# Kernel tuning notes

Measured on AMD Instinct MI355X. Metric: run time of the kernel, lower is better.

The kernel has to match this reference:

```python
import jax, jax.numpy as jnp
import numpy as np

N = 50000   # nodes
E = 800000  # edges (avg degree 16)
F = 96      # num_features
H = 96      # hidden_channels
G = 64      # graphs in batch
ALPHA = 0.5


def setup_inputs() -> dict:
    key = jax.random.key(0)
    ks = jax.random.split(key, 32)
    inp = {
        "x": jax.random.normal(ks[0], (N, F), jnp.float32),
        "edge_index": jax.random.randint(ks[1], (2, E), 0, N, dtype=jnp.int32),
        "batch": jnp.sort(jax.random.randint(ks[2], (N,), 0, G, dtype=jnp.int32)),
    }
    i = 3
    dims = [(F, H), (H, H), (H, H)]
    for l, (din, dout) in enumerate(dims, start=1):
        for tag in ("Wself", "Wsd", "Wds"):
            inp[f"{tag}{l}"] = jax.random.normal(ks[i], (din, dout), jnp.float32) * 0.05; i += 1
        for tag in ("bself", "bsd", "bds"):
            inp[f"{tag}{l}"] = jax.random.normal(ks[i], (dout,), jnp.float32) * 0.05; i += 1
    inp["lin1_w"] = jax.random.normal(ks[i], (H, 5), jnp.float32) * 0.05; i += 1
    inp["lin1_b"] = jax.random.normal(ks[i], (5,), jnp.float32) * 0.05; i += 1
    inp["lin2_w"] = jax.random.normal(ks[i], (5, 1), jnp.float32) * 0.05; i += 1
    inp["lin2_b"] = jax.random.normal(ks[i], (1,), jnp.float32) * 0.05
    return inp


def _agg_mean(x, idx_from, idx_to, n):
    # scatter-mean of x[idx_from] onto idx_to (PyG SAGEConv mean aggregation;
    # nodes with no incoming edges get 0)
    s = jax.ops.segment_sum(x[idx_from], idx_to, num_segments=n)
    c = jax.ops.segment_sum(jnp.ones((idx_to.shape[0],), x.dtype), idx_to, num_segments=n)
    return s / jnp.maximum(c, 1.0)[:, None]


def _dir_sage(x, src, dst, Wself, bself, Wsd, bsd, Wds, bds):
    n = x.shape[0]
    out_self = x @ Wself + bself
    # source_to_target: aggregate x[src] at dst; target_to_source: aggregate x[dst] at src
    out_sd = _agg_mean(x, src, dst, n) @ Wsd + bsd
    out_ds = _agg_mean(x, dst, src, n) @ Wds + bds
    return out_self + (1.0 - ALPHA) * out_sd + ALPHA * out_ds


def reference(x, edge_index, batch,
              Wself1, bself1, Wsd1, bsd1, Wds1, bds1,
              Wself2, bself2, Wsd2, bsd2, Wds2, bds2,
              Wself3, bself3, Wsd3, bsd3, Wds3, bds3,
              lin1_w, lin1_b, lin2_w, lin2_b):
    src, dst = edge_index[0], edge_index[1]
    h = jax.nn.relu(_dir_sage(x, src, dst, Wself1, bself1, Wsd1, bsd1, Wds1, bds1))
    h = jax.nn.relu(_dir_sage(h, src, dst, Wself2, bself2, Wsd2, bsd2, Wds2, bds2))
    h = jax.nn.relu(_dir_sage(h, src, dst, Wself3, bself3, Wsd3, bsd3, Wds3, bds3))
    g = jax.ops.segment_max(h, batch, num_segments=G)  # global_max_pool -> [G, H]
    g = jax.nn.relu(g @ lin1_w + lin1_b)
    return g @ lin2_w + lin2_b  # [G, 1]
```

## Files before the change

kernel.cpp:

```cpp
#include <hip/hip_runtime.h>
#include <hip/hip_bf16.h>

#define HF 96
#define GG 64
#define SB 64

typedef __attribute__((ext_vector_type(8))) short bf16x8;
typedef __attribute__((ext_vector_type(4))) float f32x4;

__device__ __forceinline__ unsigned short f2bf(float f) {
    unsigned u = __float_as_uint(f);
    unsigned r = (u + 0x7FFFu + ((u >> 16) & 1u)) >> 16;
    return (unsigned short)r;
}
__device__ __forceinline__ float bf2f(unsigned short h) {
    return __uint_as_float(((unsigned)h) << 16);
}

__global__ void count_kernel(const int* __restrict__ ei, int* __restrict__ cnt_dst,
                             int* __restrict__ cnt_src, int* __restrict__ slot_d,
                             int* __restrict__ slot_s, int E) {
    int e = blockIdx.x * blockDim.x + threadIdx.x;
    if (e >= E) return;
    int s = ei[e];
    int d = ei[E + e];
    slot_d[e] = atomicAdd(&cnt_dst[d], 1);
    slot_s[e] = atomicAdd(&cnt_src[s], 1);
}

__global__ __launch_bounds__(256) void scan_phase1(const int* __restrict__ cnt0,
                                                   const int* __restrict__ cnt1,
                                                   int* __restrict__ off0,
                                                   int* __restrict__ off1,
                                                   int* __restrict__ bsum, int N, int CH) {
    int dir = blockIdx.y;
    const int* cnt = dir ? cnt1 : cnt0;
    int* off = dir ? off1 : off0;
    int base = blockIdx.x * CH;
    int end = base + CH; if (end > N) end = N;
    __shared__ int buf[256];
    int carry = 0;
    for (int s = base; s < end; s += 256) {
        int i = s + threadIdx.x;
        int v = (i < end) ? cnt[i] : 0;
        buf[threadIdx.x] = v;
        __syncthreads();
        for (int st = 1; st < 256; st <<= 1) {
            int tv = (threadIdx.x >= st) ? buf[threadIdx.x - st] : 0;
            __syncthreads();
            buf[threadIdx.x] += tv;
            __syncthreads();
        }
        if (i < end) off[i] = carry + buf[threadIdx.x] - v;
        carry += buf[255];
        __syncthreads();
    }
    if (threadIdx.x == 0) bsum[dir * SB + blockIdx.x] = carry;
}

__global__ __launch_bounds__(64) void scan_phase2(int* __restrict__ bsum, int* __restrict__ boff,
                                                  int* __restrict__ off0, int* __restrict__ off1,
                                                  int N) {
    int dir = blockIdx.x;
    __shared__ int buf[SB];
    int v = bsum[dir * SB + threadIdx.x];
    buf[threadIdx.x] = v;
    __syncthreads();
    for (int st = 1; st < SB; st <<= 1) {
        int tv = (threadIdx.x >= st) ? buf[threadIdx.x - st] : 0;
        __syncthreads();
        buf[threadIdx.x] += tv;
        __syncthreads();
    }
    boff[dir * SB + threadIdx.x] = buf[threadIdx.x] - v;
    if (threadIdx.x == SB - 1) {
        int* off = dir ? off1 : off0;
        off[N] = buf[SB - 1];
    }
}

__global__ void scan_phase3(int* __restrict__ off0, int* __restrict__ off1,
                            const int* __restrict__ boff, int N, int CH) {
    int dir = blockIdx.y;
    int* off = dir ? off1 : off0;
    int i = blockIdx.x * 256 + threadIdx.x;
    if (i >= N) return;
    off[i] += boff[dir * SB + i / CH];
}

__global__ void fill_kernel(const int* __restrict__ ei, const int* __restrict__ off_dst,
                            const int* __restrict__ off_src, const int* __restrict__ slot_d,
                            const int* __restrict__ slot_s, int* __restrict__ nbr_dst,
                            int* __restrict__ nbr_src, int E) {
    int e = blockIdx.x * blockDim.x + threadIdx.x;
    if (e >= E) return;
    int s = ei[e];
    int d = ei[E + e];
    nbr_dst[off_dst[d] + slot_d[e]] = s;
    nbr_src[off_src[s] + slot_s[e]] = d;
}

__global__ void prep_kernel(const float* __restrict__ Wself, const float* __restrict__ Wsd,
                            const float* __restrict__ Wds, const float* __restrict__ bself,
                            const float* __restrict__ bsd, const float* __restrict__ bds,
                            unsigned short* __restrict__ Whi, unsigned short* __restrict__ Wlo,
                            float* __restrict__ bc) {
    int idx = blockIdx.x * 256 + threadIdx.x;
    if (idx < HF * 288) {
        int j = idx / 288;
        int kk = idx % 288;
        int m = kk / HF, k = kk % HF;
        const float* W = (m == 0) ? Wself : (m == 1) ? Wsd : Wds;
        float w = W[k * HF + j];
        unsigned short hi = f2bf(w);
        float rem = w - bf2f(hi);
        Whi[idx] = hi;
        Wlo[idx] = f2bf(rem);
    } else if (idx < HF * 288 + HF) {
        int j = idx - HF * 288;
        bc[j] = bself[j] + 0.5f * (bsd[j] + bds[j]);
    }
}

__global__ __launch_bounds__(256) void gather_kernel(
        const float* __restrict__ x,
        const int* __restrict__ off_dst, const int* __restrict__ nbr_dst,
        const int* __restrict__ off_src, const int* __restrict__ nbr_src,
        float* __restrict__ agg_sd, float* __restrict__ agg_ds, int N) {
    int t = blockIdx.x * blockDim.x + threadIdx.x;
    int n2 = t / 24;
    if (n2 >= 2 * N) return;
    int q = t % 24;
    int dir = (n2 >= N) ? 1 : 0;
    int n = n2 - dir * N;
    const int* off = dir ? off_src : off_dst;
    const int* nbr = dir ? nbr_src : nbr_dst;
    float* agg = dir ? agg_ds : agg_sd;

    int b = off[n], e = off[n + 1];
    const float* xq = x + q * 4;
    float4 a0 = make_float4(0.f, 0.f, 0.f, 0.f);
    float4 a1 = make_float4(0.f, 0.f, 0.f, 0.f);
    float4 a2 = make_float4(0.f, 0.f, 0.f, 0.f);
    float4 a3 = make_float4(0.f, 0.f, 0.f, 0.f);
    int i = b;
    for (; i + 4 <= e; i += 4) {
        int i0 = nbr[i + 0], i1 = nbr[i + 1], i2 = nbr[i + 2], i3 = nbr[i + 3];
        float4 v0 = *(const float4*)(xq + (long long)i0 * HF);
        float4 v1 = *(const float4*)(xq + (long long)i1 * HF);
        float4 v2 = *(const float4*)(xq + (long long)i2 * HF);
        float4 v3 = *(const float4*)(xq + (long long)i3 * HF);
        a0.x += v0.x; a0.y += v0.y; a0.z += v0.z; a0.w += v0.w;
        a1.x += v1.x; a1.y += v1.y; a1.z += v1.z; a1.w += v1.w;
        a2.x += v2.x; a2.y += v2.y; a2.z += v2.z; a2.w += v2.w;
        a3.x += v3.x; a3.y += v3.y; a3.z += v3.z; a3.w += v3.w;
    }
    for (; i < e; i++) {
        int i0 = nbr[i];
        float4 v0 = *(const float4*)(xq + (long long)i0 * HF);
        a0.x += v0.x; a0.y += v0.y; a0.z += v0.z; a0.w += v0.w;
    }
    float4 acc;
    acc.x = (a0.x + a1.x) + (a2.x + a3.x);
    acc.y = (a0.y + a1.y) + (a2.y + a3.y);
    acc.z = (a0.z + a1.z) + (a2.z + a3.z);
    acc.w = (a0.w + a1.w) + (a2.w + a3.w);
    float inv = 0.5f / fmaxf((float)(e - b), 1.0f);
    acc.x *= inv; acc.y *= inv; acc.z *= inv; acc.w *= inv;
    *(float4*)(agg + (long long)n * HF + q * 4) = acc;
}

#define LPAD 48
__global__ __launch_bounds__(256) void sage_mfma(
        const float* __restrict__ x, const float* __restrict__ agg_sd,
        const float* __restrict__ agg_ds,
        const unsigned short* __restrict__ Whi_g, const unsigned short* __restrict__ Wlo_g,
        const float* __restrict__ bc,
        float* __restrict__ out, int N) {
    __shared__ __align__(16) unsigned short Ahi[128 * LPAD];
    __shared__ __align__(16) unsigned short Alo[128 * LPAD];
    __shared__ __align__(16) unsigned short Whi[96 * LPAD];
    __shared__ __align__(16) unsigned short Wlo[96 * LPAD];

    const int tx = threadIdx.x;
    const int lane = tx & 63;
    const int wid = tx >> 6;
    const int wr = (wid >> 1) * 64;
    const int wc = (wid & 1) * 48;
    const int m = lane & 15;
    const int quad = lane >> 4;
    const int row0 = blockIdx.x * 128;

    const int arow = tx >> 1;
    const int ahalf = tx & 1;
    int argr = row0 + arow; if (argr > N - 1) argr = N - 1;

    f32x4 acc[4][3];
#pragma unroll
    for (int rt = 0; rt < 4; rt++)
#pragma unroll
        for (int ct = 0; ct < 3; ct++) acc[rt][ct] = (f32x4){0.f, 0.f, 0.f, 0.f};

    for (int kt = 0; kt < 9; kt++) {
        const float* A = (kt < 3) ? x : (kt < 6) ? agg_sd : agg_ds;
        const int koff = (kt % 3) * 32;
        const int kglob = kt * 32;

        {
            const float* Ar = A + (long long)argr * HF + koff + ahalf * 16;
            float4 v0 = *(const float4*)(Ar + 0);
            float4 v1 = *(const float4*)(Ar + 4);
            float4 v2 = *(const float4*)(Ar + 8);
            float4 v3 = *(const float4*)(Ar + 12);
            float f[16] = {v0.x, v0.y, v0.z, v0.w, v1.x, v1.y, v1.z, v1.w,
                           v2.x, v2.y, v2.z, v2.w, v3.x, v3.y, v3.z, v3.w};
            bf16x8 hv0, lv0, hv1, lv1;
#pragma unroll
            for (int i = 0; i < 8; i++) {
                unsigned short h = f2bf(f[i]);
                hv0[i] = (short)h;
                lv0[i] = (short)f2bf(f[i] - bf2f(h));
            }
#pragma unroll
            for (int i = 0; i < 8; i++) {
                unsigned short h = f2bf(f[8 + i]);
                hv1[i] = (short)h;
                lv1[i] = (short)f2bf(f[8 + i] - bf2f(h));
            }
            int base = arow * LPAD + ahalf * 16;
            *(bf16x8*)&Ahi[base + 0] = hv0;
            *(bf16x8*)&Ahi[base + 8] = hv1;
            *(bf16x8*)&Alo[base + 0] = lv0;
            *(bf16x8*)&Alo[base + 8] = lv1;
        }
        for (int s = tx; s < 384; s += 256) {
            int j = s >> 2, q2 = s & 3;
            long long go = (long long)j * 288 + kglob + q2 * 8;
            *(bf16x8*)&Whi[j * LPAD + q2 * 8] = *(const bf16x8*)(Whi_g + go);
            *(bf16x8*)&Wlo[j * LPAD + q2 * 8] = *(const bf16x8*)(Wlo_g + go);
        }
        __syncthreads();

        bf16x8 ah[4], al[4], bh[3], bl[3];
#pragma unroll
        for (int rt = 0; rt < 4; rt++) {
            int r = (wr + rt * 16 + m) * LPAD + quad * 8;
            ah[rt] = *(const bf16x8*)&Ahi[r];
            al[rt] = *(const bf16x8*)&Alo[r];
        }
#pragma unroll
        for (int ct = 0; ct < 3; ct++) {
            int r = (wc + ct * 16 + m) * LPAD + quad * 8;
            bh[ct] = *(const bf16x8*)&Whi[r];
            bl[ct] = *(const bf16x8*)&Wlo[r];
        }
#pragma unroll
        for (int rt = 0; rt < 4; rt++)
#pragma unroll
            for (int ct = 0; ct < 3; ct++) {
                acc[rt][ct] = __builtin_amdgcn_mfma_f32_16x16x32_bf16(ah[rt], bh[ct], acc[rt][ct], 0, 0, 0);
                acc[rt][ct] = __builtin_amdgcn_mfma_f32_16x16x32_bf16(ah[rt], bl[ct], acc[rt][ct], 0, 0, 0);
                acc[rt][ct] = __builtin_amdgcn_mfma_f32_16x16x32_bf16(al[rt], bh[ct], acc[rt][ct], 0, 0, 0);
            }
        __syncthreads();
    }

#pragma unroll
    for (int ct = 0; ct < 3; ct++) {
        int col = wc + ct * 16 + m;
        float bcv = bc[col];
#pragma unroll
        for (int rt = 0; rt < 4; rt++) {
#pragma unroll
            for (int reg = 0; reg < 4; reg++) {
                int r = row0 + wr + rt * 16 + quad * 4 + reg;
                if (r < N) out[(long long)r * HF + col] = fmaxf(acc[rt][ct][reg] + bcv, 0.f);
            }
        }
    }
}

#define POOL_CHUNK 128
__global__ void pool_kernel(const float* __restrict__ h, const int* __restrict__ batch,
                            unsigned* __restrict__ g, int N) {
    int j = threadIdx.x;
    if (j >= HF) return;
    int n0 = blockIdx.x * POOL_CHUNK;
    int end = n0 + POOL_CHUNK;
    if (end > N) end = N;
    float cur = 0.0f;
    int curb = -1;
    for (int n = n0; n < end; n++) {
        int b = batch[n];
        float v = h[(long long)n * HF + j];
        if (b != curb) {
            if (curb >= 0) atomicMax(&g[curb * HF + j], __float_as_uint(cur));
            curb = b;
            cur = v;
        } else {
            cur = fmaxf(cur, v);
        }
    }
    if (curb >= 0) atomicMax(&g[curb * HF + j], __float_as_uint(cur));
}

__global__ void mlp_kernel(const unsigned* __restrict__ g, const float* __restrict__ lin1_w,
                           const float* __restrict__ lin1_b, const float* __restrict__ lin2_w,
                           const float* __restrict__ lin2_b, float* __restrict__ out) {
    int gi = threadIdx.x;
    if (gi >= GG) return;
    float h5[5];
#pragma unroll
    for (int hh = 0; hh < 5; hh++) {
        float acc = lin1_b[hh];
#pragma unroll 8
        for (int k = 0; k < HF; k++)
            acc = fmaf(__uint_as_float(g[gi * HF + k]), lin1_w[k * 5 + hh], acc);
        h5[hh] = fmaxf(acc, 0.0f);
    }
    float o = lin2_b[0];
#pragma unroll
    for (int hh = 0; hh < 5; hh++) o = fmaf(h5[hh], lin2_w[hh * 1 + 0], o);
    out[gi] = o;
}

extern "C" void kernel_launch(void* const* d_in, const int* in_sizes, int n_in,
                              void* d_out, int out_size, void* d_ws, size_t ws_size,
                              hipStream_t stream) {
    const float* x     = (const float*)d_in[0];
    const int*   ei    = (const int*)d_in[1];
    const int*   batch = (const int*)d_in[2];
    const float* W[3][3];
    const float* B[3][3];
    for (int l = 0; l < 3; l++) {
        for (int t = 0; t < 3; t++) W[l][t] = (const float*)d_in[3 + l * 6 + t];
        for (int t = 0; t < 3; t++) B[l][t] = (const float*)d_in[3 + l * 6 + 3 + t];
    }
    const float* lin1_w = (const float*)d_in[21];
    const float* lin1_b = (const float*)d_in[22];
    const float* lin2_w = (const float*)d_in[23];
    const float* lin2_b = (const float*)d_in[24];

    const int N = in_sizes[0] / HF;
    const int E = in_sizes[1] / 2;

    float* hA      = (float*)d_ws;
    float* hB      = hA + (long long)N * HF;
    float* agg_sd  = hB + (long long)N * HF;
    float* agg_ds  = agg_sd + (long long)N * HF;
    int*   cnt_dst = (int*)(agg_ds + (long long)N * HF);
    int*   cnt_src = cnt_dst + N;
    int*   off_dst = cnt_src + N;
    int*   off_src = off_dst + (N + 1);
    int*   nbr_dst = off_src + (N + 1);
    int*   nbr_src = nbr_dst + E;
    int*   slot_d  = nbr_src + E;
    int*   slot_s  = slot_d + E;
    int*   bsum    = slot_s + E;
    int*   boff    = bsum + 2 * SB;
    float* bc3     = (float*)(boff + 2 * SB);
    uintptr_t p = (uintptr_t)(bc3 + 3 * HF);
    p = (p + 15) & ~(uintptr_t)15;
    unsigned short* Whi3 = (unsigned short*)p;
    unsigned short* Wlo3 = Whi3 + 3 * HF * 288;
    uintptr_t p2 = (uintptr_t)(Wlo3 + 3 * HF * 288);
    p2 = (p2 + 15) & ~(uintptr_t)15;
    unsigned* g = (unsigned*)p2;

    hipMemsetAsync(cnt_dst, 0, (size_t)2 * N * sizeof(int), stream);
    hipMemsetAsync(g, 0, (size_t)GG * HF * sizeof(unsigned), stream);

    const int prep_blocks = (HF * 288 + HF + 255) / 256;
    for (int l = 0; l < 3; l++)
        prep_kernel<<<prep_blocks, 256, 0, stream>>>(
            W[l][0], W[l][1], W[l][2], B[l][0], B[l][1], B[l][2],
            Whi3 + (long long)l * HF * 288, Wlo3 + (long long)l * HF * 288, bc3 + l * HF);

    const int CH = (N + SB - 1) / SB;
    count_kernel<<<(E + 255) / 256, 256, 0, stream>>>(ei, cnt_dst, cnt_src, slot_d, slot_s, E);
    scan_phase1<<<dim3(SB, 2), 256, 0, stream>>>(cnt_dst, cnt_src, off_dst, off_src, bsum, N, CH);
    scan_phase2<<<2, SB, 0, stream>>>(bsum, boff, off_dst, off_src, N);
    scan_phase3<<<dim3((N + 255) / 256, 2), 256, 0, stream>>>(off_dst, off_src, boff, N, CH);
    fill_kernel<<<(E + 255) / 256, 256, 0, stream>>>(ei, off_dst, off_src,
                                                     slot_d, slot_s, nbr_dst, nbr_src, E);

    const long long gather_threads = (long long)2 * N * 24;
    const int gather_blocks = (int)((gather_threads + 255) / 256);
    const int gemm_blocks = (N + 127) / 128;
    const int pool_blocks = (N + POOL_CHUNK - 1) / POOL_CHUNK;

    const float* cur_in = x;
    float* outs[3] = { hA, hB, hA };
    for (int l = 0; l < 3; l++) {
        gather_kernel<<<gather_blocks, 256, 0, stream>>>(
            cur_in, off_dst, nbr_dst, off_src, nbr_src, agg_sd, agg_ds, N);
        sage_mfma<<<gemm_blocks, 256, 0, stream>>>(
            cur_in, agg_sd, agg_ds,
            Whi3 + (long long)l * HF * 288, Wlo3 + (long long)l * HF * 288,
            bc3 + l * HF, outs[l], N);
        cur_in = outs[l];
    }

    pool_kernel<<<pool_blocks, 128, 0, stream>>>(outs[2], batch, g, N);
    mlp_kernel<<<1, 64, 0, stream>>>(g, lin1_w, lin1_b, lin2_w, lin2_b, (float*)d_out);
}
```

Before: 568.4 us.

## Remap gather threads to one node per lane with feature-slice blocks

The gather kernel changes from 24 threads per node, each summing a float4 slice, to one thread per (node, direction) pair. Blocks are split into 8 feature slices of 12 floats, each slice loaded as three float4s per neighbor. This cuts repeated neighbor-index and offset loads per node and lets consecutive blocks share slices of the same rows in cache. The cost is uncoalesced per-lane row accesses and lane divergence from differing degrees within a wavefront.

```diff
diff --git a/kernel.cpp b/kernel.cpp
--- a/kernel.cpp
+++ b/kernel.cpp
@@ -127,47 +127,60 @@
         const int* __restrict__ off_dst, const int* __restrict__ nbr_dst,
         const int* __restrict__ off_src, const int* __restrict__ nbr_src,
         float* __restrict__ agg_sd, float* __restrict__ agg_ds, int N) {
-    int t = blockIdx.x * blockDim.x + threadIdx.x;
-    int n2 = t / 24;
-    if (n2 >= 2 * N) return;
-    int q = t % 24;
-    int dir = (n2 >= N) ? 1 : 0;
-    int n = n2 - dir * N;
+    const int t8 = blockIdx.x & 7;
+    int pair = (blockIdx.x >> 3) * 256 + threadIdx.x;
+    if (pair >= 2 * N) return;
+    int dir = (pair >= N) ? 1 : 0;
+    int n = pair - dir * N;
     const int* off = dir ? off_src : off_dst;
     const int* nbr = dir ? nbr_src : nbr_dst;
     float* agg = dir ? agg_ds : agg_sd;
 
     int b = off[n], e = off[n + 1];
-    const float* xq = x + q * 4;
+    const float* xt = x + t8 * 12;
     float4 a0 = make_float4(0.f, 0.f, 0.f, 0.f);
     float4 a1 = make_float4(0.f, 0.f, 0.f, 0.f);
     float4 a2 = make_float4(0.f, 0.f, 0.f, 0.f);
-    float4 a3 = make_float4(0.f, 0.f, 0.f, 0.f);
+    float4 c0 = make_float4(0.f, 0.f, 0.f, 0.f);
+    float4 c1 = make_float4(0.f, 0.f, 0.f, 0.f);
+    float4 c2 = make_float4(0.f, 0.f, 0.f, 0.f);
     int i = b;
-    for (; i + 4 <= e; i += 4) {
-        int i0 = nbr[i + 0], i1 = nbr[i + 1], i2 = nbr[i + 2], i3 = nbr[i + 3];
-        float4 v0 = *(const float4*)(xq + (long long)i0 * HF);
-        float4 v1 = *(const float4*)(xq + (long long)i1 * HF);
-        float4 v2 = *(const float4*)(xq + (long long)i2 * HF);
-        float4 v3 = *(const float4*)(xq + (long long)i3 * HF);
-        a0.x += v0.x; a0.y += v0.y; a0.z += v0.z; a0.w += v0.w;
-        a1.x += v1.x; a1.y += v1.y; a1.z += v1.z; a1.w += v1.w;
-        a2.x += v2.x; a2.y += v2.y; a2.z += v2.z; a2.w += v2.w;
-        a3.x += v3.x; a3.y += v3.y; a3.z += v3.z; a3.w += v3.w;
-    }
-    for (; i < e; i++) {
-        int i0 = nbr[i];
-        float4 v0 = *(const float4*)(xq + (long long)i0 * HF);
-        a0.x += v0.x; a0.y += v0.y; a0.z += v0.z; a0.w += v0.w;
-    }
-    float4 acc;
-    acc.x = (a0.x + a1.x) + (a2.x + a3.x);
-    acc.y = (a0.y + a1.y) + (a2.y + a3.y);
-    acc.z = (a0.z + a1.z) + (a2.z + a3.z);
-    acc.w = (a0.w + a1.w) + (a2.w + a3.w);
+    for (; i + 2 <= e; i += 2) {
+        long long r0 = (long long)nbr[i] * HF;
+        long long r1 = (long long)nbr[i + 1] * HF;
+        float4 u0 = *(const float4*)(xt + r0 + 0);
+        float4 u1 = *(const float4*)(xt + r0 + 4);
+        float4 u2 = *(const float4*)(xt + r0 + 8);
+        float4 w0 = *(const float4*)(xt + r1 + 0);
+        float4 w1 = *(const float4*)(xt + r1 + 4);
+        float4 w2 = *(const float4*)(xt + r1 + 8);
+        a0.x += u0.x; a0.y += u0.y; a0.z += u0.z; a0.w += u0.w;
+        a1.x += u1.x; a1.y += u1.y; a1.z += u1.z; a1.w += u1.w;
+        a2.x += u2.x; a2.y += u2.y; a2.z += u2.z; a2.w += u2.w;
+        c0.x += w0.x; c0.y += w0.y; c0.z += w0.z; c0.w += w0.w;
+        c1.x += w1.x; c1.y += w1.y; c1.z += w1.z; c1.w += w1.w;
+        c2.x += w2.x; c2.y += w2.y; c2.z += w2.z; c2.w += w2.w;
+    }
+    if (i < e) {
+        long long r0 = (long long)nbr[i] * HF;
+        float4 u0 = *(const float4*)(xt + r0 + 0);
+        float4 u1 = *(const float4*)(xt + r0 + 4);
+        float4 u2 = *(const float4*)(xt + r0 + 8);
+        a0.x += u0.x; a0.y += u0.y; a0.z += u0.z; a0.w += u0.w;
+        a1.x += u1.x; a1.y += u1.y; a1.z += u1.z; a1.w += u1.w;
+        a2.x += u2.x; a2.y += u2.y; a2.z += u2.z; a2.w += u2.w;
+    }
     float inv = 0.5f / fmaxf((float)(e - b), 1.0f);
-    acc.x *= inv; acc.y *= inv; acc.z *= inv; acc.w *= inv;
-    *(float4*)(agg + (long long)n * HF + q * 4) = acc;
+    a0.x = (a0.x + c0.x) * inv; a0.y = (a0.y + c0.y) * inv;
+    a0.z = (a0.z + c0.z) * inv; a0.w = (a0.w + c0.w) * inv;
+    a1.x = (a1.x + c1.x) * inv; a1.y = (a1.y + c1.y) * inv;
+    a1.z = (a1.z + c1.z) * inv; a1.w = (a1.w + c1.w) * inv;
+    a2.x = (a2.x + c2.x) * inv; a2.y = (a2.y + c2.y) * inv;
+    a2.z = (a2.z + c2.z) * inv; a2.w = (a2.w + c2.w) * inv;
+    float* po = agg + (long long)n * HF + t8 * 12;
+    *(float4*)(po + 0) = a0;
+    *(float4*)(po + 4) = a1;
+    *(float4*)(po + 8) = a2;
 }
 
 #define LPAD 48
@@ -384,8 +397,7 @@
     fill_kernel<<<(E + 255) / 256, 256, 0, stream>>>(ei, off_dst, off_src,
                                                      slot_d, slot_s, nbr_dst, nbr_src, E);
 
-    const long long gather_threads = (long long)2 * N * 24;
-    const int gather_blocks = (int)((gather_threads + 255) / 256);
+    const int gather_blocks = ((2 * N + 255) / 256) * 8;
     const int gemm_blocks = (N + 127) / 128;
     const int pool_blocks = (N + POOL_CHUNK - 1) / POOL_CHUNK;
 
```

Result: slower. 1.278 ms (+124.9%).
